# Kernel tuning notes

Measured on AMD Instinct MI355X. Metric: run time of the kernel, lower is better.

## Reference

```python
import jax, jax.numpy as jnp
import numpy as np

B, C, G = 8, 64, 65536
IN_DIM, OUT_DIM = 64, 64
SLOPE = 0.1


def setup_inputs() -> dict:
    key = jax.random.key(0)
    ks = jax.random.split(key, 5)
    features = jax.random.normal(ks[0], (B, C, G), dtype=jnp.float32)
    # Conv2d(in*2, out, 1, bias=False) weights, squeezed to [out, in*2]
    W0 = jax.random.normal(ks[1], (OUT_DIM, IN_DIM * 2), dtype=jnp.float32) * (1.0 / np.sqrt(IN_DIM * 2))
    W1 = jax.random.normal(ks[2], (OUT_DIM, OUT_DIM * 2), dtype=jnp.float32) * (1.0 / np.sqrt(OUT_DIM * 2))
    W2 = jax.random.normal(ks[3], (OUT_DIM, OUT_DIM * 2), dtype=jnp.float32) * (1.0 / np.sqrt(OUT_DIM * 2))
    W3 = jax.random.normal(ks[4], (OUT_DIM, OUT_DIM * 2), dtype=jnp.float32) * (1.0 / np.sqrt(OUT_DIM * 2))
    return {"features": features, "W0": W0, "W1": W1, "W2": W2, "W3": W3}


def _layer(x, W):
    # x: [B, C, G]; tile the first group's features and build (x, x - x0)
    x0 = x[:, :, :1]                               # [B, C, 1]
    h = jnp.concatenate([x, x - x0], axis=1)       # [B, 2C, G]
    # 1x1 conv == pointwise linear over channels
    y = jnp.einsum("oc,bcg->bog", W, h)            # [B, O, G]
    return jax.nn.leaky_relu(y, negative_slope=SLOPE)


def reference(features, W0, W1, W2, W3):
    x = features
    for W in (W0, W1, W2, W3):
        x = _layer(x, W)
    return jnp.max(x, axis=-1)                     # [B, O]
```

## Files before the change

### kernel.cpp

```cpp
#include <hip/hip_runtime.h>


#define G_TOT 65536

typedef _Float16 hf2 __attribute__((ext_vector_type(2)));
typedef _Float16 hf4 __attribute__((ext_vector_type(4)));
typedef _Float16 hf8 __attribute__((ext_vector_type(8)));
typedef float float2_ __attribute__((ext_vector_type(2)));
typedef float float4_ __attribute__((ext_vector_type(4)));

static __device__ __forceinline__ hf2 pkh(float x, float y) {
    return __builtin_bit_cast(hf2, __builtin_amdgcn_cvt_pkrtz(x, y));
}


__global__ __launch_bounds__(256) void ge_prep(
    const float* __restrict__ feat,
    const float* __restrict__ W0, const float* __restrict__ W1,
    const float* __restrict__ W2, const float* __restrict__ W3,
    float* __restrict__ ws)
{
    const int tid = threadIdx.x;
    const int blk = blockIdx.x;
    __shared__ float lw[64][129];
    __shared__ float x0[2][64];

    if (blk == 8) {
        unsigned* maxenc = (unsigned*)(ws + 18432);
        maxenc[tid] = 0u; maxenc[tid + 256] = 0u;
        _Float16* wf = (_Float16*)ws;
        for (int ci = tid; ci < 8192; ci += 256) {
            int f = ci >> 8, ln = (ci >> 2) & 63, h2 = ci & 3;
            int l = f >> 3, mt = (f >> 1) & 3, pr = f & 1;
            int o = (mt << 4) + (ln & 15);
            int c = (pr << 5) + ((h2 >> 1) << 4) + ((ln >> 4) << 2) + ((h2 & 1) << 1);
            const float* Wl = (l == 0) ? W0 : (l == 1) ? W1 : (l == 2) ? W2 : W3;
            float a0 = Wl[o * 128 + c]     + Wl[o * 128 + 64 + c];
            float a1 = Wl[o * 128 + c + 1] + Wl[o * 128 + 64 + c + 1];
            *(hf2*)&wf[ci << 1] = pkh(a0, a1);
        }
        return;
    }

    const int b = blk;
    if (tid < 64) x0[0][tid] = feat[(size_t)(b * 64 + tid) * G_TOT];
    float* nbias = ws + 16384;
    for (int l = 0; l < 4; ++l) {
        const float* Wl = (l == 0) ? W0 : (l == 1) ? W1 : (l == 2) ? W2 : W3;
        for (int i = tid; i < 64 * 128; i += 256) lw[i >> 7][i & 127] = Wl[i];
        __syncthreads();
        if (tid < 64) {
            const int o = tid;
            const float* src = x0[l & 1];
            float s1 = 0.f, s2 = 0.f;
            for (int c = 0; c < 64; ++c) {
                float xv = src[c];
                s1 += lw[o][c] * xv;
                s2 += lw[o][64 + c] * xv;
            }
            nbias[b * 256 + l * 64 + o] = -s2;
            x0[(l & 1) ^ 1][o] = fmaxf(s1, 0.1f * s1);
        }
        __syncthreads();
    }
}

#define COMPUTE_TILE(BF)                                                              \
    _Pragma("unroll")                                                                 \
    for (int l = 0; l < 4; ++l) {                                                     \
        float4_ acc[4];                                                               \
        _Pragma("unroll")                                                             \
        for (int mt = 0; mt < 4; ++mt) {                                              \
            if (l < 3) acc[mt] = *(const float4_*)&lbias[(l << 6) + (mt << 4) + (q << 2)]; \
            else       acc[mt] = float4_{0.f, 0.f, 0.f, 0.f};                         \
        }                                                                             \
        _Pragma("unroll")                                                             \
        for (int mt = 0; mt < 4; ++mt) {                                              \
            _Pragma("unroll")                                                         \
            for (int pr = 0; pr < 2; ++pr) {                                          \
                union { hf8 h8; hf4 h4[2]; } ua;                                      \
                ua.h8 = wfr[l][mt][pr];                                               \
                acc[mt] = __builtin_amdgcn_mfma_f32_16x16x16f16(ua.h4[0], BF[(pr << 1) + 0], acc[mt], 0, 0, 0); \
                acc[mt] = __builtin_amdgcn_mfma_f32_16x16x16f16(ua.h4[1], BF[(pr << 1) + 1], acc[mt], 0, 0, 0); \
            }                                                                         \
        }                                                                             \
        if (l < 3) {                                                                  \
            _Pragma("unroll")                                                         \
            for (int mt = 0; mt < 4; ++mt) {                                          \
                union { hf2 h2[2]; hf4 h4; } u;                                       \
                u.h2[0] = pkh(acc[mt][0], acc[mt][1]);                                \
                u.h2[1] = pkh(acc[mt][2], acc[mt][3]);                                \
                hf4 h = u.h4;                                                         \
                h = __builtin_elementwise_max(h, h * k01);                            \
                BF[mt] = h;                                                           \
            }                                                                         \
        } else {                                                                      \
            _Pragma("unroll")                                                         \
            for (int mt = 0; mt < 4; ++mt)                                            \
                _Pragma("unroll")                                                     \
                for (int j = 0; j < 4; ++j)                                           \
                    rmax[mt][j] = fmaxf(rmax[mt][j], acc[mt][j]);                     \
        }                                                                             \
    }

__global__ __launch_bounds__(256, 2) void ge_main(
    const float* __restrict__ feat,
    const float* __restrict__ ws_wf,
    const float* __restrict__ nbias,
    unsigned* __restrict__ maxenc)
{
    __shared__ float lbias[256];
    __shared__ float blockmax[4][64];
    const int tid = threadIdx.x;
    const int b = blockIdx.x >> 6;
    const int w = tid >> 6, lane = tid & 63, q = lane >> 4, n = lane & 15;
    const int g0 = ((blockIdx.x & 63) << 10) + (w << 8);

    const float* Xbase = feat + (size_t)b * 64 * G_TOT + (size_t)(q << 2) * G_TOT
                       + (size_t)g0 + (size_t)(n << 1);

    float2_ buf[16];
#pragma unroll
    for (int kf = 0; kf < 4; ++kf)
#pragma unroll
        for (int r = 0; r < 4; ++r)
            buf[kf * 4 + r] = *(const float2_*)&Xbase[(size_t)((kf << 4) + r) * G_TOT];

    hf8 wfr[4][4][2];
    {
        const hf8* wp = (const hf8*)ws_wf;
#pragma unroll
        for (int l = 0; l < 4; ++l)
#pragma unroll
            for (int mt = 0; mt < 4; ++mt)
#pragma unroll
                for (int pr = 0; pr < 2; ++pr)
                    wfr[l][mt][pr] = wp[((((((l << 2) + mt) << 1) + pr)) << 6) + lane];
    }

    lbias[tid] = nbias[(b << 8) + tid];
    __syncthreads();

    float rmax[4][4];
#pragma unroll
    for (int mt = 0; mt < 4; ++mt)
#pragma unroll
        for (int j = 0; j < 4; ++j) rmax[mt][j] = -__builtin_inff();

    const hf4 k01 = { (_Float16)0.1f, (_Float16)0.1f, (_Float16)0.1f, (_Float16)0.1f };

#pragma unroll 1
    for (int grp = 0; grp < 8; ++grp) {
        hf4 bfA[4], bfB[4];
#pragma unroll
        for (int kf = 0; kf < 4; ++kf) {
            union { hf2 h2[2]; hf4 h4; } ua, ub;
            ua.h2[0] = pkh(buf[kf * 4 + 0][0], buf[kf * 4 + 1][0]);
            ua.h2[1] = pkh(buf[kf * 4 + 2][0], buf[kf * 4 + 3][0]);
            ub.h2[0] = pkh(buf[kf * 4 + 0][1], buf[kf * 4 + 1][1]);
            ub.h2[1] = pkh(buf[kf * 4 + 2][1], buf[kf * 4 + 3][1]);
            bfA[kf] = ua.h4;
            bfB[kf] = ub.h4;
        }
        if (grp < 7) {
            const float* Xp = Xbase + ((grp + 1) << 5);
#pragma unroll
            for (int kf = 0; kf < 4; ++kf)
#pragma unroll
                for (int r = 0; r < 4; ++r)
                    buf[kf * 4 + r] = *(const float2_*)&Xp[(size_t)((kf << 4) + r) * G_TOT];
        }
        COMPUTE_TILE(bfA)
        COMPUTE_TILE(bfB)
    }

#pragma unroll
    for (int mt = 0; mt < 4; ++mt)
#pragma unroll
        for (int j = 0; j < 4; ++j) {
            float v = rmax[mt][j];
            v = fmaxf(v, __shfl_xor(v, 1, 64));
            v = fmaxf(v, __shfl_xor(v, 2, 64));
            v = fmaxf(v, __shfl_xor(v, 4, 64));
            v = fmaxf(v, __shfl_xor(v, 8, 64));
            rmax[mt][j] = v;
        }
    if (n == 0) {
#pragma unroll
        for (int mt = 0; mt < 4; ++mt)
#pragma unroll
            for (int j = 0; j < 4; ++j)
                blockmax[w][(mt << 4) + (q << 2) + j] = rmax[mt][j];
    }
    __syncthreads();
    if (tid < 64) {
        float v = fmaxf(fmaxf(blockmax[0][tid], blockmax[1][tid]),
                        fmaxf(blockmax[2][tid], blockmax[3][tid]));
        unsigned s = __float_as_uint(v);
        unsigned enc = (s & 0x80000000u) ? ~s : (s | 0x80000000u);
        atomicMax(&maxenc[b * 64 + tid], enc);
    }
}

__global__ void ge_final(const unsigned* __restrict__ maxenc,
                         const float* __restrict__ nbias,
                         float* __restrict__ out)
{
    int i = threadIdx.x;
    if (i < 512) {
        unsigned u = maxenc[i];
        unsigned s = (u & 0x80000000u) ? (u ^ 0x80000000u) : ~u;
        float v = __uint_as_float(s) + nbias[((i >> 6) << 8) + 192 + (i & 63)];
        out[i] = fmaxf(v, 0.1f * v);
    }
}

extern "C" void kernel_launch(void* const* d_in, const int* in_sizes, int n_in,
                              void* d_out, int out_size, void* d_ws, size_t ws_size,
                              hipStream_t stream) {
    const float* feat = (const float*)d_in[0];
    const float* W0 = (const float*)d_in[1];
    const float* W1 = (const float*)d_in[2];
    const float* W2 = (const float*)d_in[3];
    const float* W3 = (const float*)d_in[4];
    float* ws = (float*)d_ws;
    unsigned* maxenc = (unsigned*)(ws + 18432);

    ge_prep<<<9, 256, 0, stream>>>(feat, W0, W1, W2, W3, ws);
    ge_main<<<512, 256, 0, stream>>>(feat, ws, ws + 16384, maxenc);
    ge_final<<<1, 512, 0, stream>>>(maxenc, ws + 16384, (float*)d_out);
}
```

Baseline: 222.4 us.

## Stage feature tiles through LDS with float4 coalesced loads

Replaces the per-lane float2 global loads, which were scattered across 16 rows per wave, with a cooperative block-wide float4 load of a 64x128 tile into padded shared memory. Each wave then reads its MFMA operand columns from LDS. The goal is wider, better-coalesced global reads that fetch full contiguous 512-byte row segments. In exchange it adds two barriers per tile, extra LDS traffic, and about 34 KB of shared memory per block, which may reduce occupancy.

After: 278.8 us. +25.4%, slower.

```diff
diff --git a/kernel.cpp b/kernel.cpp
--- a/kernel.cpp
+++ b/kernel.cpp
@@ -6,7 +6,6 @@
 typedef _Float16 hf2 __attribute__((ext_vector_type(2)));
 typedef _Float16 hf4 __attribute__((ext_vector_type(4)));
 typedef _Float16 hf8 __attribute__((ext_vector_type(8)));
-typedef float float2_ __attribute__((ext_vector_type(2)));
 typedef float float4_ __attribute__((ext_vector_type(4)));
 
 static __device__ __forceinline__ hf2 pkh(float x, float y) {
@@ -109,22 +108,22 @@
     const float* __restrict__ nbias,
     unsigned* __restrict__ maxenc)
 {
+    __shared__ __align__(16) float stg[64][132];
     __shared__ float lbias[256];
     __shared__ float blockmax[4][64];
     const int tid = threadIdx.x;
     const int b = blockIdx.x >> 6;
     const int w = tid >> 6, lane = tid & 63, q = lane >> 4, n = lane & 15;
-    const int g0 = ((blockIdx.x & 63) << 10) + (w << 8);
-
-    const float* Xbase = feat + (size_t)b * 64 * G_TOT + (size_t)(q << 2) * G_TOT
-                       + (size_t)g0 + (size_t)(n << 1);
-
-    float2_ buf[16];
-#pragma unroll
-    for (int kf = 0; kf < 4; ++kf)
-#pragma unroll
-        for (int r = 0; r < 4; ++r)
-            buf[kf * 4 + r] = *(const float2_*)&Xbase[(size_t)((kf << 4) + r) * G_TOT];
+
+    const int srow = (w << 4) + (lane >> 5);
+    const int scol = (lane & 31) << 2;
+    const float* Sbase = feat + (size_t)b * 64 * G_TOT
+                       + (size_t)((blockIdx.x & 63) << 10) + scol;
+
+    float4_ sbuf[8];
+#pragma unroll
+    for (int i = 0; i < 8; ++i)
+        sbuf[i] = *(const float4_*)&Sbase[(size_t)(srow + (i << 1)) * G_TOT];
 
     hf8 wfr[4][4][2];
     {
@@ -139,7 +138,6 @@
     }
 
     lbias[tid] = nbias[(b << 8) + tid];
-    __syncthreads();
 
     float rmax[4][4];
 #pragma unroll
@@ -150,28 +148,46 @@
     const hf4 k01 = { (_Float16)0.1f, (_Float16)0.1f, (_Float16)0.1f, (_Float16)0.1f };
 
 #pragma unroll 1
-    for (int grp = 0; grp < 8; ++grp) {
-        hf4 bfA[4], bfB[4];
-#pragma unroll
-        for (int kf = 0; kf < 4; ++kf) {
-            union { hf2 h2[2]; hf4 h4; } ua, ub;
-            ua.h2[0] = pkh(buf[kf * 4 + 0][0], buf[kf * 4 + 1][0]);
-            ua.h2[1] = pkh(buf[kf * 4 + 2][0], buf[kf * 4 + 3][0]);
-            ub.h2[0] = pkh(buf[kf * 4 + 0][1], buf[kf * 4 + 1][1]);
-            ub.h2[1] = pkh(buf[kf * 4 + 2][1], buf[kf * 4 + 3][1]);
-            bfA[kf] = ua.h4;
-            bfB[kf] = ub.h4;
-        }
-        if (grp < 7) {
-            const float* Xp = Xbase + ((grp + 1) << 5);
-#pragma unroll
-            for (int kf = 0; kf < 4; ++kf)
-#pragma unroll
-                for (int r = 0; r < 4; ++r)
-                    buf[kf * 4 + r] = *(const float2_*)&Xp[(size_t)((kf << 4) + r) * G_TOT];
-        }
-        COMPUTE_TILE(bfA)
-        COMPUTE_TILE(bfB)
+    for (int p = 0; p < 8; ++p) {
+        __syncthreads();
+#pragma unroll
+        for (int i = 0; i < 8; ++i)
+            *(float4_*)&stg[(w << 4) + (i << 1) + (lane >> 5)][scol] = sbuf[i];
+        __syncthreads();
+        if (p < 7) {
+            const float* Sp = Sbase + ((p + 1) << 7);
+#pragma unroll
+            for (int i = 0; i < 8; ++i)
+                sbuf[i] = *(const float4_*)&Sp[(size_t)(srow + (i << 1)) * G_TOT];
+        }
+        {
+            hf4 bfA[4];
+#pragma unroll
+            for (int kf = 0; kf < 4; ++kf) {
+                float f0 = stg[(kf << 4) + (q << 2) + 0][(w << 5) + n];
+                float f1 = stg[(kf << 4) + (q << 2) + 1][(w << 5) + n];
+                float f2 = stg[(kf << 4) + (q << 2) + 2][(w << 5) + n];
+                float f3 = stg[(kf << 4) + (q << 2) + 3][(w << 5) + n];
+                union { hf2 h2[2]; hf4 h4; } u;
+                u.h2[0] = pkh(f0, f1); u.h2[1] = pkh(f2, f3);
+                bfA[kf] = u.h4;
+            }
+            COMPUTE_TILE(bfA)
+        }
+        {
+            hf4 bfB[4];
+#pragma unroll
+            for (int kf = 0; kf < 4; ++kf) {
+                float f0 = stg[(kf << 4) + (q << 2) + 0][(w << 5) + 16 + n];
+                float f1 = stg[(kf << 4) + (q << 2) + 1][(w << 5) + 16 + n];
+                float f2 = stg[(kf << 4) + (q << 2) + 2][(w << 5) + 16 + n];
+                float f3 = stg[(kf << 4) + (q << 2) + 3][(w << 5) + 16 + n];
+                union { hf2 h2[2]; hf4 h4; } u;
+                u.h2[0] = pkh(f0, f1); u.h2[1] = pkh(f2, f3);
+                bfB[kf] = u.h4;
+            }
+            COMPUTE_TILE(bfB)
+        }
     }
 
 #pragma unroll
```
